# Performance work log

Hardware: AMD Instinct MI355X
Metric: run time of the kernel (lower is better)

## Reference

```python
import math
import jax, jax.numpy as jnp
import numpy as np

DIM = 1024
N_HEADS = 16
N_KV_HEADS = 4
HEAD_DIM = 64
WINDOW = 512
EPS = 1e-6
B, S = 2, 2048

def _alibi_slopes(n_heads):
    def pow2(n):
        r = 2.0 ** (-8.0 / n)
        return np.array([r ** (i + 1) for i in range(n)], dtype=np.float32)
    if math.log2(n_heads).is_integer():
        return pow2(n_heads)
    m = 2 ** math.floor(math.log2(n_heads))
    return np.concatenate([pow2(m), pow2(2 * m)[::2][: n_heads - m]])

def _rmsnorm(x, w, eps=EPS):
    var = jnp.mean(x * x, axis=-1, keepdims=True)
    return x * jax.lax.rsqrt(var + eps) * w

def setup_inputs() -> dict:
    key = jax.random.key(0)
    ks = jax.random.split(key, 8)
    x = jax.random.normal(ks[0], (B, S, DIM), dtype=jnp.float32)
    wq = 0.02 * jax.random.normal(ks[1], (N_HEADS * HEAD_DIM, DIM), dtype=jnp.float32)
    wk = 0.02 * jax.random.normal(ks[2], (N_KV_HEADS * HEAD_DIM, DIM), dtype=jnp.float32)
    wv = 0.02 * jax.random.normal(ks[3], (N_KV_HEADS * HEAD_DIM, DIM), dtype=jnp.float32)
    wo = 0.02 * jax.random.normal(ks[4], (DIM, N_HEADS * HEAD_DIM), dtype=jnp.float32)
    q_norm_w = jnp.ones((N_HEADS * HEAD_DIM,), dtype=jnp.float32)
    k_norm_w = jnp.ones((N_KV_HEADS * HEAD_DIM,), dtype=jnp.float32)
    return {"x": x, "wq": wq, "wk": wk, "wv": wv, "wo": wo,
            "q_norm_w": q_norm_w, "k_norm_w": k_norm_w}

def reference(x, wq, wk, wv, wo, q_norm_w, k_norm_w):
    bsz, seqlen, _ = x.shape
    repeats = N_HEADS // N_KV_HEADS
    xq = _rmsnorm(x @ wq.T, q_norm_w)
    xk = _rmsnorm(x @ wk.T, k_norm_w)
    xv = x @ wv.T
    # [b, h, s, d]
    q = xq.reshape(bsz, seqlen, N_HEADS, HEAD_DIM).transpose(0, 2, 1, 3)
    k = xk.reshape(bsz, seqlen, N_KV_HEADS, HEAD_DIM).transpose(0, 2, 1, 3)
    v = xv.reshape(bsz, seqlen, N_KV_HEADS, HEAD_DIM).transpose(0, 2, 1, 3)
    k = jnp.repeat(k, repeats, axis=1)
    v = jnp.repeat(v, repeats, axis=1)
    pos = jnp.arange(seqlen)
    rel = pos[None, :] - pos[:, None]  # [s_q, s_k], key - query
    slopes = jnp.asarray(_alibi_slopes(N_HEADS))
    bias = slopes[:, None, None] * rel[None].astype(x.dtype)  # [h, s, s]
    masked = (rel > 0) | (rel < -WINDOW)  # causal + sliding window
    bias = jnp.where(masked[None], -jnp.inf, bias)
    scale = 1.0 / math.sqrt(HEAD_DIM)
    scores = jnp.einsum('bhqd,bhkd->bhqk', q, k) * scale + bias[None]
    probs = jax.nn.softmax(scores, axis=-1)
    y = jnp.einsum('bhqk,bhkd->bhqd', probs, v)
    y = y.transpose(0, 2, 1, 3).reshape(bsz, seqlen, N_HEADS * HEAD_DIM)
    return y @ wo.T
```

## Files before the change

### kernel.cpp

```cpp
#include <hip/hip_runtime.h>

typedef unsigned short u16;
typedef unsigned int u32;

typedef __bf16 bf16x8 __attribute__((ext_vector_type(8)));
typedef float f32x4 __attribute__((ext_vector_type(4)));

__device__ __forceinline__ u16 f2bf(float f) {
  u32 u = __builtin_bit_cast(u32, f);
  u32 r = (u + 0x7fffu + ((u >> 16) & 1u)) >> 16;
  return (u16)r;
}
__device__ __forceinline__ float bf2f(u16 v) {
  u32 u = (u32)v << 16;
  return __builtin_bit_cast(float, u);
}

__global__ __launch_bounds__(256)
void cvt_all_kernel(const float* __restrict__ x, const float* __restrict__ wq,
                    const float* __restrict__ wk, const float* __restrict__ wv,
                    const float* __restrict__ wo, u16* __restrict__ x_bf,
                    u16* __restrict__ wcat_bf, u16* __restrict__ wo_bf) {
  int t = blockIdx.x * 256 + threadIdx.x;
  const float* src;
  u16* dst;
  if (t < 1048576) {
    src = x; dst = x_bf;
  } else if (t < 1310720) {
    src = wq; dst = wcat_bf; t -= 1048576;
  } else if (t < 1376256) {
    src = wk; dst = wcat_bf + 1048576; t -= 1310720;
  } else if (t < 1441792) {
    src = wv; dst = wcat_bf + 1310720; t -= 1376256;
  } else {
    src = wo; dst = wo_bf; t -= 1441792;
  }
  const int i = t * 4;
  float4 v = *(const float4*)(src + i);
  uint2 p;
  p.x = (u32)f2bf(v.x) | ((u32)f2bf(v.y) << 16);
  p.y = (u32)f2bf(v.z) | ((u32)f2bf(v.w) << 16);
  *(uint2*)(dst + i) = p;
}

template <typename OutT>
__global__ __launch_bounds__(256)
void gemm_bt_kernel(const u16* __restrict__ A, const u16* __restrict__ B,
                    OutT* __restrict__ C, int M, int N, int K) {
  __shared__ u16 As[64 * 64];
  __shared__ u16 Bs[128 * 64];
  const int tid = threadIdx.x;
  const int lane = tid & 63;
  const int wave = tid >> 6;
  const int wm = (wave >> 1) * 32;
  const int wn = (wave & 1) * 64;
  const int l15 = lane & 15;
  const int quad = lane >> 4;
  const int sw = l15 & 7;
  const size_t bm = (size_t)blockIdx.y * 64;
  const size_t bn = (size_t)blockIdx.x * 128;

  f32x4 acc[2][4];
#pragma unroll
  for (int i = 0; i < 2; ++i)
#pragma unroll
    for (int j = 0; j < 4; ++j) acc[i][j] = f32x4{0.f, 0.f, 0.f, 0.f};

  const int ra0 = tid >> 3, ba0 = tid & 7;
  const int ra1 = (tid + 256) >> 3, ba1 = tid & 7;
  const u16* Ap0 = A + (bm + ra0) * (size_t)K + ba0 * 8;
  const u16* Ap1 = A + (bm + ra1) * (size_t)K + ba1 * 8;
  const u16* Bp0 = B + (bn + ra0) * (size_t)K + ba0 * 8;
  const u16* Bp1 = B + (bn + ra1) * (size_t)K + ba1 * 8;
  const u16* Bp2 = B + (bn + ra0 + 64) * (size_t)K + ba0 * 8;
  const u16* Bp3 = B + (bn + ra1 + 64) * (size_t)K + ba1 * 8;
  const int wa0 = ra0 * 64 + ((ba0 ^ (ra0 & 7)) * 8);
  const int wa1 = ra1 * 64 + ((ba1 ^ (ra1 & 7)) * 8);
  const int wb2 = (ra0 + 64) * 64 + ((ba0 ^ (ra0 & 7)) * 8);
  const int wb3 = (ra1 + 64) * 64 + ((ba1 ^ (ra1 & 7)) * 8);

  uint4 a0 = *(const uint4*)Ap0, a1 = *(const uint4*)Ap1;
  uint4 b0 = *(const uint4*)Bp0, b1 = *(const uint4*)Bp1;
  uint4 b2 = *(const uint4*)Bp2, b3 = *(const uint4*)Bp3;

  for (int k0 = 0; k0 < K; k0 += 64) {
    __syncthreads();
    *(uint4*)(&As[wa0]) = a0;
    *(uint4*)(&As[wa1]) = a1;
    *(uint4*)(&Bs[wa0]) = b0;
    *(uint4*)(&Bs[wa1]) = b1;
    *(uint4*)(&Bs[wb2]) = b2;
    *(uint4*)(&Bs[wb3]) = b3;
    __syncthreads();
    const int kn = (k0 + 64 < K) ? k0 + 64 : 0;
    a0 = *(const uint4*)(Ap0 + kn);
    a1 = *(const uint4*)(Ap1 + kn);
    b0 = *(const uint4*)(Bp0 + kn);
    b1 = *(const uint4*)(Bp1 + kn);
    b2 = *(const uint4*)(Bp2 + kn);
    b3 = *(const uint4*)(Bp3 + kn);
#pragma unroll
    for (int h = 0; h < 2; ++h) {
      const int cb = (quad + 4 * h);
      bf16x8 af[2], bfr[4];
#pragma unroll
      for (int i = 0; i < 2; ++i)
        af[i] = *(const bf16x8*)(&As[(wm + i * 16 + l15) * 64 + ((cb ^ sw) * 8)]);
#pragma unroll
      for (int j = 0; j < 4; ++j)
        bfr[j] = *(const bf16x8*)(&Bs[(wn + j * 16 + l15) * 64 + ((cb ^ sw) * 8)]);
#pragma unroll
      for (int i = 0; i < 2; ++i)
#pragma unroll
        for (int j = 0; j < 4; ++j)
          acc[i][j] = __builtin_amdgcn_mfma_f32_16x16x32_bf16(af[i], bfr[j], acc[i][j], 0, 0, 0);
    }
  }

  const int rq = quad * 4;
#pragma unroll
  for (int i = 0; i < 2; ++i) {
#pragma unroll
    for (int r = 0; r < 4; ++r) {
      OutT* crow = C + (bm + wm + i * 16 + rq + r) * (size_t)N + bn + wn + l15;
#pragma unroll
      for (int j = 0; j < 4; ++j) {
        if constexpr (sizeof(OutT) == 2)
          crow[j * 16] = f2bf(acc[i][j][r]);
        else
          crow[j * 16] = acc[i][j][r];
      }
    }
  }
}

__global__ __launch_bounds__(256)
void norm_vtrans_kernel(u16* __restrict__ qkv, const float* __restrict__ qw,
                        const float* __restrict__ kw, u16* __restrict__ vt) {
  __shared__ u16 shmem[64 * 72];
  const int bid = blockIdx.x;
  const int tid = threadIdx.x;
  if (bid < 4096) {
    float* red = (float*)shmem;
    u16* row = qkv + (size_t)bid * 1536;
    uint2 pk = *(const uint2*)(row + tid * 4);
    float v0 = bf2f((u16)pk.x), v1 = bf2f((u16)(pk.x >> 16));
    float v2 = bf2f((u16)pk.y), v3 = bf2f((u16)(pk.y >> 16));
    float ss = v0 * v0 + v1 * v1 + v2 * v2 + v3 * v3;
#pragma unroll
    for (int off = 32; off > 0; off >>= 1) ss += __shfl_down(ss, off);
    if ((tid & 63) == 0) red[tid >> 6] = ss;
    __syncthreads();
    float tot = red[0] + red[1] + red[2] + red[3];
    float rn = rsqrtf(tot * (1.0f / 1024.0f) + 1e-6f);
    float4 w = *(const float4*)(qw + tid * 4);
    uint2 po;
    po.x = (u32)f2bf(v0 * rn * w.x) | ((u32)f2bf(v1 * rn * w.y) << 16);
    po.y = (u32)f2bf(v2 * rn * w.z) | ((u32)f2bf(v3 * rn * w.w) << 16);
    *(uint2*)(row + tid * 4) = po;
    if (tid < 64) {
      uint2 kp = *(const uint2*)(row + 1024 + tid * 4);
      float k0 = bf2f((u16)kp.x), k1 = bf2f((u16)(kp.x >> 16));
      float k2 = bf2f((u16)kp.y), k3 = bf2f((u16)(kp.y >> 16));
      float sk = k0 * k0 + k1 * k1 + k2 * k2 + k3 * k3;
#pragma unroll
      for (int off = 32; off > 0; off >>= 1) sk += __shfl_down(sk, off);
      float tk = __shfl(sk, 0);
      float rk = rsqrtf(tk * (1.0f / 256.0f) + 1e-6f);
      float4 w2 = *(const float4*)(kw + tid * 4);
      uint2 ko;
      ko.x = (u32)f2bf(k0 * rk * w2.x) | ((u32)f2bf(k1 * rk * w2.y) << 16);
      ko.y = (u32)f2bf(k2 * rk * w2.z) | ((u32)f2bf(k3 * rk * w2.w) << 16);
      *(uint2*)(row + 1024 + tid * 4) = ko;
    }
  } else {
    const int e = bid - 4096;
    const int t0 = (e & 31) * 64, kvh = (e >> 5) & 3, b = e >> 7;
    u16(*tile)[72] = (u16(*)[72])shmem;
    const int r = tid >> 2, c16 = (tid & 3) * 16;
    const u16* src = qkv + (size_t)(b * 2048 + t0 + r) * 1536 + 1280 + kvh * 64 + c16;
    *(uint4*)&tile[r][c16] = *(const uint4*)src;
    *(uint4*)&tile[r][c16 + 8] = *(const uint4*)(src + 8);
    __syncthreads();
    const int d = tid >> 2, t16 = (tid & 3) * 16;
    u16 o[16];
#pragma unroll
    for (int j = 0; j < 16; ++j) o[j] = tile[t16 + j][d];
    u16* dst = vt + (size_t)((b * 4 + kvh) * 64 + d) * 2048 + t0 + t16;
    *(uint4*)dst = *(uint4*)&o[0];
    *(uint4*)(dst + 8) = *(uint4*)&o[8];
  }
}

__global__ __launch_bounds__(512)
void attn_kernel(const u16* __restrict__ qkvbf, const u16* __restrict__ vt,
                 u16* __restrict__ ybf) {
  __shared__ u16 Ks[64 * 72];
  __shared__ u16 Vts[64 * 72];
  __shared__ u16 Ps[128 * 72];
  const int qt = blockIdx.x, h = blockIdx.y, b = blockIdx.z;
  const int kvh = h >> 2, q0 = qt * 128;
  const int tid = threadIdx.x, lane = tid & 63, w = tid >> 6;
  const int l15 = lane & 15, quad = lane >> 4;

  const u16* qrow = qkvbf + (size_t)(b * 2048 + q0 + w * 16 + l15) * 1536 + h * 64 + quad * 8;
  const bf16x8 qf0 = *(const bf16x8*)qrow;
  const bf16x8 qf1 = *(const bf16x8*)(qrow + 32);

  const int sr = tid >> 3, sc = (tid & 7) * 8;
  const u16* kbase = qkvbf + (size_t)(b * 2048 + sr) * 1536 + 1024 + kvh * 64 + sc;
  const u16* vbase = vt + (size_t)((b * 4 + kvh) * 64 + sr) * 2048 + sc;

  f32x4 O[4];
#pragma unroll
  for (int jd = 0; jd < 4; ++jd) O[jd] = f32x4{0.f, 0.f, 0.f, 0.f};
  float m_i = -1e30f, l_i = 0.f;
  const float LOG2E = 1.44269504f;
  const float sc2 = 0.125f * LOG2E;
  const float slope2 = exp2f(-0.5f * (float)(h + 1)) * LOG2E;
  const int c_lo = (q0 >= 512) ? (q0 - 512) : 0;
  const int c_hi = q0 + 64;
  const int myq_lo = q0 + w * 16;
  const int myq_hi = myq_lo + 15;
  const int myq = myq_lo + l15;

  uint4 kr = *(const uint4*)(kbase + (size_t)c_lo * 1536);
  uint4 vr = *(const uint4*)(vbase + c_lo);

  for (int c = c_lo; c <= c_hi; c += 64) {
    __syncthreads();
    *(uint4*)&Ks[sr * 72 + sc] = kr;
    *(uint4*)&Vts[sr * 72 + sc] = vr;
    __syncthreads();
    {
      const int cn = (c + 64 <= c_hi) ? c + 64 : c_lo;
      kr = *(const uint4*)(kbase + (size_t)cn * 1536);
      vr = *(const uint4*)(vbase + cn);
    }

    if (c > myq_hi || c + 63 < myq_lo - 512) continue;

    f32x4 st[4];
#pragma unroll
    for (int i = 0; i < 4; ++i) {
      bf16x8 a0 = *(const bf16x8*)&Ks[(i * 16 + l15) * 72 + quad * 8];
      bf16x8 a1 = *(const bf16x8*)&Ks[(i * 16 + l15) * 72 + 32 + quad * 8];
      f32x4 z = f32x4{0.f, 0.f, 0.f, 0.f};
      z = __builtin_amdgcn_mfma_f32_16x16x32_bf16(a0, qf0, z, 0, 0, 0);
      st[i] = __builtin_amdgcn_mfma_f32_16x16x32_bf16(a1, qf1, z, 0, 0, 0);
    }

    float sv[4][4];
    float rm = -1e30f;
    const bool interior = (c + 63 <= myq_lo) && (c + 512 >= myq_hi);
    if (interior) {
#pragma unroll
      for (int i = 0; i < 4; ++i)
#pragma unroll
        for (int r = 0; r < 4; ++r) {
          const int key = c + i * 16 + quad * 4 + r;
          float val = st[i][r] * sc2 + slope2 * (float)(key - myq);
          sv[i][r] = val;
          rm = fmaxf(rm, val);
        }
    } else {
#pragma unroll
      for (int i = 0; i < 4; ++i)
#pragma unroll
        for (int r = 0; r < 4; ++r) {
          const int key = c + i * 16 + quad * 4 + r;
          const int rel = key - myq;
          float val = (rel > 0 || rel < -512) ? -1e30f
                                              : st[i][r] * sc2 + slope2 * (float)rel;
          sv[i][r] = val;
          rm = fmaxf(rm, val);
        }
    }
    rm = fmaxf(rm, __shfl_xor(rm, 16));
    rm = fmaxf(rm, __shfl_xor(rm, 32));
    const float mn = fmaxf(m_i, rm);
    const float alpha = exp2f(m_i - mn);
    float ls = 0.f;
#pragma unroll
    for (int i = 0; i < 4; ++i) {
      float p0 = exp2f(sv[i][0] - mn);
      float p1 = exp2f(sv[i][1] - mn);
      float p2 = exp2f(sv[i][2] - mn);
      float p3 = exp2f(sv[i][3] - mn);
      ls += (p0 + p1) + (p2 + p3);
      uint2 pw;
      pw.x = (u32)f2bf(p0) | ((u32)f2bf(p1) << 16);
      pw.y = (u32)f2bf(p2) | ((u32)f2bf(p3) << 16);
      *(uint2*)&Ps[(w * 16 + l15) * 72 + i * 16 + quad * 4] = pw;
    }
    ls += __shfl_xor(ls, 16);
    ls += __shfl_xor(ls, 32);
    l_i = l_i * alpha + ls;
    m_i = mn;

    float ar[4];
#pragma unroll
    for (int r = 0; r < 4; ++r) ar[r] = __shfl(alpha, quad * 4 + r);
#pragma unroll
    for (int jd = 0; jd < 4; ++jd)
#pragma unroll
      for (int r = 0; r < 4; ++r) O[jd][r] *= ar[r];

    bf16x8 pf0 = *(const bf16x8*)&Ps[(w * 16 + l15) * 72 + quad * 8];
    bf16x8 pf1 = *(const bf16x8*)&Ps[(w * 16 + l15) * 72 + 32 + quad * 8];
#pragma unroll
    for (int jd = 0; jd < 4; ++jd) {
      bf16x8 v0 = *(const bf16x8*)&Vts[(jd * 16 + l15) * 72 + quad * 8];
      bf16x8 v1 = *(const bf16x8*)&Vts[(jd * 16 + l15) * 72 + 32 + quad * 8];
      O[jd] = __builtin_amdgcn_mfma_f32_16x16x32_bf16(pf0, v0, O[jd], 0, 0, 0);
      O[jd] = __builtin_amdgcn_mfma_f32_16x16x32_bf16(pf1, v1, O[jd], 0, 0, 0);
    }
  }

  float lr[4];
#pragma unroll
  for (int r = 0; r < 4; ++r) lr[r] = __shfl(l_i, quad * 4 + r);
#pragma unroll
  for (int r = 0; r < 4; ++r) {
    const float inv = 1.0f / lr[r];
    u16* orow = ybf + (size_t)(b * 2048 + q0 + w * 16 + quad * 4 + r) * 1024 + h * 64 + l15;
#pragma unroll
    for (int jd = 0; jd < 4; ++jd) orow[jd * 16] = f2bf(O[jd][r] * inv);
  }
}

extern "C" void kernel_launch(void* const* d_in, const int* in_sizes, int n_in,
                              void* d_out, int out_size, void* d_ws, size_t ws_size,
                              hipStream_t stream) {
  const float* x = (const float*)d_in[0];
  const float* wq = (const float*)d_in[1];
  const float* wk = (const float*)d_in[2];
  const float* wv = (const float*)d_in[3];
  const float* wo = (const float*)d_in[4];
  const float* qnw = (const float*)d_in[5];
  const float* knw = (const float*)d_in[6];
  float* out = (float*)d_out;
  char* ws = (char*)d_ws;

  u16* x_bf = (u16*)(ws);
  u16* wcat_bf = (u16*)(ws + 8388608);
  u16* wo_bf = (u16*)(ws + 11534336);
  u16* qkv_bf = (u16*)(ws + 13631488);
  u16* vt_bf = (u16*)(ws + 26214400);
  u16* y_bf = (u16*)(ws + 28311552);

  cvt_all_kernel<<<6656, 256, 0, stream>>>(x, wq, wk, wv, wo, x_bf, wcat_bf, wo_bf);

  gemm_bt_kernel<u16><<<dim3(12, 64), 256, 0, stream>>>(x_bf, wcat_bf, qkv_bf, 4096, 1536, 1024);
  norm_vtrans_kernel<<<4352, 256, 0, stream>>>(qkv_bf, qnw, knw, vt_bf);
  attn_kernel<<<dim3(16, 16, 2), 512, 0, stream>>>(qkv_bf, vt_bf, y_bf);
  gemm_bt_kernel<float><<<dim3(8, 64), 256, 0, stream>>>(y_bf, wo_bf, out, 4096, 1024, 1024);
}
```

Measured before the change: 160.3 us.

## Double-buffer shared memory tiles in GEMM and attention kernels

Both the GEMM and attention kernels now keep two LDS buffers for the operand tiles and use one barrier per iteration instead of two. The next tile is fetched from global memory, the current buffer is consumed by MFMA, and the fetched data is then written into the other buffer. The aim is to cut barrier overhead and overlap loads with compute. In exchange, LDS use doubles, which may lower occupancy, particularly for the attention kernel.

```diff
diff --git a/kernel.cpp b/kernel.cpp
--- a/kernel.cpp
+++ b/kernel.cpp
@@ -47,8 +47,8 @@
 __global__ __launch_bounds__(256)
 void gemm_bt_kernel(const u16* __restrict__ A, const u16* __restrict__ B,
                     OutT* __restrict__ C, int M, int N, int K) {
-  __shared__ u16 As[64 * 64];
-  __shared__ u16 Bs[128 * 64];
+  __shared__ u16 As[2][64 * 64];
+  __shared__ u16 Bs[2][128 * 64];
   const int tid = threadIdx.x;
   const int lane = tid & 63;
   const int wave = tid >> 6;
@@ -79,42 +79,58 @@
   const int wb2 = (ra0 + 64) * 64 + ((ba0 ^ (ra0 & 7)) * 8);
   const int wb3 = (ra1 + 64) * 64 + ((ba1 ^ (ra1 & 7)) * 8);
 
-  uint4 a0 = *(const uint4*)Ap0, a1 = *(const uint4*)Ap1;
-  uint4 b0 = *(const uint4*)Bp0, b1 = *(const uint4*)Bp1;
-  uint4 b2 = *(const uint4*)Bp2, b3 = *(const uint4*)Bp3;
-
+  {
+    uint4 a0 = *(const uint4*)Ap0, a1 = *(const uint4*)Ap1;
+    uint4 b0 = *(const uint4*)Bp0, b1 = *(const uint4*)Bp1;
+    uint4 b2 = *(const uint4*)Bp2, b3 = *(const uint4*)Bp3;
+    *(uint4*)(&As[0][wa0]) = a0;
+    *(uint4*)(&As[0][wa1]) = a1;
+    *(uint4*)(&Bs[0][wa0]) = b0;
+    *(uint4*)(&Bs[0][wa1]) = b1;
+    *(uint4*)(&Bs[0][wb2]) = b2;
+    *(uint4*)(&Bs[0][wb3]) = b3;
+  }
+  __syncthreads();
+
+  int cur = 0;
   for (int k0 = 0; k0 < K; k0 += 64) {
-    __syncthreads();
-    *(uint4*)(&As[wa0]) = a0;
-    *(uint4*)(&As[wa1]) = a1;
-    *(uint4*)(&Bs[wa0]) = b0;
-    *(uint4*)(&Bs[wa1]) = b1;
-    *(uint4*)(&Bs[wb2]) = b2;
-    *(uint4*)(&Bs[wb3]) = b3;
-    __syncthreads();
     const int kn = (k0 + 64 < K) ? k0 + 64 : 0;
-    a0 = *(const uint4*)(Ap0 + kn);
-    a1 = *(const uint4*)(Ap1 + kn);
-    b0 = *(const uint4*)(Bp0 + kn);
-    b1 = *(const uint4*)(Bp1 + kn);
-    b2 = *(const uint4*)(Bp2 + kn);
-    b3 = *(const uint4*)(Bp3 + kn);
+    uint4 a0 = *(const uint4*)(Ap0 + kn);
+    uint4 a1 = *(const uint4*)(Ap1 + kn);
+    uint4 b0 = *(const uint4*)(Bp0 + kn);
+    uint4 b1 = *(const uint4*)(Bp1 + kn);
+    uint4 b2 = *(const uint4*)(Bp2 + kn);
+    uint4 b3 = *(const uint4*)(Bp3 + kn);
+
+    const u16* Asc = As[cur];
+    const u16* Bsc = Bs[cur];
 #pragma unroll
     for (int h = 0; h < 2; ++h) {
-      const int cb = (quad + 4 * h);
+      const int cb = quad + 4 * h;
       bf16x8 af[2], bfr[4];
 #pragma unroll
       for (int i = 0; i < 2; ++i)
-        af[i] = *(const bf16x8*)(&As[(wm + i * 16 + l15) * 64 + ((cb ^ sw) * 8)]);
+        af[i] = *(const bf16x8*)(&Asc[(wm + i * 16 + l15) * 64 + ((cb ^ sw) * 8)]);
 #pragma unroll
       for (int j = 0; j < 4; ++j)
-        bfr[j] = *(const bf16x8*)(&Bs[(wn + j * 16 + l15) * 64 + ((cb ^ sw) * 8)]);
+        bfr[j] = *(const bf16x8*)(&Bsc[(wn + j * 16 + l15) * 64 + ((cb ^ sw) * 8)]);
 #pragma unroll
       for (int i = 0; i < 2; ++i)
 #pragma unroll
         for (int j = 0; j < 4; ++j)
           acc[i][j] = __builtin_amdgcn_mfma_f32_16x16x32_bf16(af[i], bfr[j], acc[i][j], 0, 0, 0);
     }
+
+    u16* Asn = As[cur ^ 1];
+    u16* Bsn = Bs[cur ^ 1];
+    *(uint4*)(&Asn[wa0]) = a0;
+    *(uint4*)(&Asn[wa1]) = a1;
+    *(uint4*)(&Bsn[wa0]) = b0;
+    *(uint4*)(&Bsn[wa1]) = b1;
+    *(uint4*)(&Bsn[wb2]) = b2;
+    *(uint4*)(&Bsn[wb3]) = b3;
+    __syncthreads();
+    cur ^= 1;
   }
 
   const int rq = quad * 4;
@@ -195,8 +211,8 @@
 __global__ __launch_bounds__(512)
 void attn_kernel(const u16* __restrict__ qkvbf, const u16* __restrict__ vt,
                  u16* __restrict__ ybf) {
-  __shared__ u16 Ks[64 * 72];
-  __shared__ u16 Vts[64 * 72];
+  __shared__ u16 Ks[2][64 * 72];
+  __shared__ u16 Vts[2][64 * 72];
   __shared__ u16 Ps[128 * 72];
   const int qt = blockIdx.x, h = blockIdx.y, b = blockIdx.z;
   const int kvh = h >> 2, q0 = qt * 128;
@@ -224,97 +240,104 @@
   const int myq_hi = myq_lo + 15;
   const int myq = myq_lo + l15;
 
-  uint4 kr = *(const uint4*)(kbase + (size_t)c_lo * 1536);
-  uint4 vr = *(const uint4*)(vbase + c_lo);
-
+  {
+    uint4 kr = *(const uint4*)(kbase + (size_t)c_lo * 1536);
+    uint4 vr = *(const uint4*)(vbase + c_lo);
+    *(uint4*)&Ks[0][sr * 72 + sc] = kr;
+    *(uint4*)&Vts[0][sr * 72 + sc] = vr;
+  }
+  __syncthreads();
+
+  int cur = 0;
   for (int c = c_lo; c <= c_hi; c += 64) {
+    const int cn = (c + 64 <= c_hi) ? c + 64 : c_lo;
+    uint4 kr = *(const uint4*)(kbase + (size_t)cn * 1536);
+    uint4 vr = *(const uint4*)(vbase + cn);
+
+    if (!(c > myq_hi || c + 63 < myq_lo - 512)) {
+      const u16* Kc = Ks[cur];
+      const u16* Vc = Vts[cur];
+      f32x4 st[4];
+#pragma unroll
+      for (int i = 0; i < 4; ++i) {
+        bf16x8 a0 = *(const bf16x8*)&Kc[(i * 16 + l15) * 72 + quad * 8];
+        bf16x8 a1 = *(const bf16x8*)&Kc[(i * 16 + l15) * 72 + 32 + quad * 8];
+        f32x4 z = f32x4{0.f, 0.f, 0.f, 0.f};
+        z = __builtin_amdgcn_mfma_f32_16x16x32_bf16(a0, qf0, z, 0, 0, 0);
+        st[i] = __builtin_amdgcn_mfma_f32_16x16x32_bf16(a1, qf1, z, 0, 0, 0);
+      }
+
+      float sv[4][4];
+      float rm = -1e30f;
+      const bool interior = (c + 63 <= myq_lo) && (c + 512 >= myq_hi);
+      if (interior) {
+#pragma unroll
+        for (int i = 0; i < 4; ++i)
+#pragma unroll
+          for (int r = 0; r < 4; ++r) {
+            const int key = c + i * 16 + quad * 4 + r;
+            float val = st[i][r] * sc2 + slope2 * (float)(key - myq);
+            sv[i][r] = val;
+            rm = fmaxf(rm, val);
+          }
+      } else {
+#pragma unroll
+        for (int i = 0; i < 4; ++i)
+#pragma unroll
+          for (int r = 0; r < 4; ++r) {
+            const int key = c + i * 16 + quad * 4 + r;
+            const int rel = key - myq;
+            float val = (rel > 0 || rel < -512) ? -1e30f
+                                                : st[i][r] * sc2 + slope2 * (float)rel;
+            sv[i][r] = val;
+            rm = fmaxf(rm, val);
+          }
+      }
+      rm = fmaxf(rm, __shfl_xor(rm, 16));
+      rm = fmaxf(rm, __shfl_xor(rm, 32));
+      const float mn = fmaxf(m_i, rm);
+      const float alpha = exp2f(m_i - mn);
+      float ls = 0.f;
+#pragma unroll
+      for (int i = 0; i < 4; ++i) {
+        float p0 = exp2f(sv[i][0] - mn);
+        float p1 = exp2f(sv[i][1] - mn);
+        float p2 = exp2f(sv[i][2] - mn);
+        float p3 = exp2f(sv[i][3] - mn);
+        ls += (p0 + p1) + (p2 + p3);
+        uint2 pw;
+        pw.x = (u32)f2bf(p0) | ((u32)f2bf(p1) << 16);
+        pw.y = (u32)f2bf(p2) | ((u32)f2bf(p3) << 16);
+        *(uint2*)&Ps[(w * 16 + l15) * 72 + i * 16 + quad * 4] = pw;
+      }
+      ls += __shfl_xor(ls, 16);
+      ls += __shfl_xor(ls, 32);
+      l_i = l_i * alpha + ls;
+      m_i = mn;
+
+      float ar[4];
+#pragma unroll
+      for (int r = 0; r < 4; ++r) ar[r] = __shfl(alpha, quad * 4 + r);
+#pragma unroll
+      for (int jd = 0; jd < 4; ++jd)
+#pragma unroll
+        for (int r = 0; r < 4; ++r) O[jd][r] *= ar[r];
+
+      bf16x8 pf0 = *(const bf16x8*)&Ps[(w * 16 + l15) * 72 + quad * 8];
+      bf16x8 pf1 = *(const bf16x8*)&Ps[(w * 16 + l15) * 72 + 32 + quad * 8];
+#pragma unroll
+      for (int jd = 0; jd < 4; ++jd) {
+        bf16x8 v0 = *(const bf16x8*)&Vc[(jd * 16 + l15) * 72 + quad * 8];
+        bf16x8 v1 = *(const bf16x8*)&Vc[(jd * 16 + l15) * 72 + 32 + quad * 8];
+        O[jd] = __builtin_amdgcn_mfma_f32_16x16x32_bf16(pf0, v0, O[jd], 0, 0, 0);
+        O[jd] = __builtin_amdgcn_mfma_f32_16x16x32_bf16(pf1, v1, O[jd], 0, 0, 0);
+      }
+    }
+
+    *(uint4*)&Ks[cur ^ 1][sr * 72 + sc] = kr;
+    *(uint4*)&Vts[cur ^ 1][sr * 72 + sc] = vr;
     __syncthreads();
-    *(uint4*)&Ks[sr * 72 + sc] = kr;
-    *(uint4*)&Vts[sr * 72 + sc] = vr;
-    __syncthreads();
-    {
-      const int cn = (c + 64 <= c_hi) ? c + 64 : c_lo;
-      kr = *(const uint4*)(kbase + (size_t)cn * 1536);
-      vr = *(const uint4*)(vbase + cn);
-    }
-
-    if (c > myq_hi || c + 63 < myq_lo - 512) continue;
-
-    f32x4 st[4];
-#pragma unroll
-    for (int i = 0; i < 4; ++i) {
-      bf16x8 a0 = *(const bf16x8*)&Ks[(i * 16 + l15) * 72 + quad * 8];
-      bf16x8 a1 = *(const bf16x8*)&Ks[(i * 16 + l15) * 72 + 32 + quad * 8];
-      f32x4 z = f32x4{0.f, 0.f, 0.f, 0.f};
-      z = __builtin_amdgcn_mfma_f32_16x16x32_bf16(a0, qf0, z, 0, 0, 0);
-      st[i] = __builtin_amdgcn_mfma_f32_16x16x32_bf16(a1, qf1, z, 0, 0, 0);
-    }
-
-    float sv[4][4];
-    float rm = -1e30f;
-    const bool interior = (c + 63 <= myq_lo) && (c + 512 >= myq_hi);
-    if (interior) {
-#pragma unroll
-      for (int i = 0; i < 4; ++i)
-#pragma unroll
-        for (int r = 0; r < 4; ++r) {
-          const int key = c + i * 16 + quad * 4 + r;
-          float val = st[i][r] * sc2 + slope2 * (float)(key - myq);
-          sv[i][r] = val;
-          rm = fmaxf(rm, val);
-        }
-    } else {
-#pragma unroll
-      for (int i = 0; i < 4; ++i)
-#pragma unroll
-        for (int r = 0; r < 4; ++r) {
-          const int key = c + i * 16 + quad * 4 + r;
-          const int rel = key - myq;
-          float val = (rel > 0 || rel < -512) ? -1e30f
-                                              : st[i][r] * sc2 + slope2 * (float)rel;
-          sv[i][r] = val;
-          rm = fmaxf(rm, val);
-        }
-    }
-    rm = fmaxf(rm, __shfl_xor(rm, 16));
-    rm = fmaxf(rm, __shfl_xor(rm, 32));
-    const float mn = fmaxf(m_i, rm);
-    const float alpha = exp2f(m_i - mn);
-    float ls = 0.f;
-#pragma unroll
-    for (int i = 0; i < 4; ++i) {
-      float p0 = exp2f(sv[i][0] - mn);
-      float p1 = exp2f(sv[i][1] - mn);
-      float p2 = exp2f(sv[i][2] - mn);
-      float p3 = exp2f(sv[i][3] - mn);
-      ls += (p0 + p1) + (p2 + p3);
-      uint2 pw;
-      pw.x = (u32)f2bf(p0) | ((u32)f2bf(p1) << 16);
-      pw.y = (u32)f2bf(p2) | ((u32)f2bf(p3) << 16);
-      *(uint2*)&Ps[(w * 16 + l15) * 72 + i * 16 + quad * 4] = pw;
-    }
-    ls += __shfl_xor(ls, 16);
-    ls += __shfl_xor(ls, 32);
-    l_i = l_i * alpha + ls;
-    m_i = mn;
-
-    float ar[4];
-#pragma unroll
-    for (int r = 0; r < 4; ++r) ar[r] = __shfl(alpha, quad * 4 + r);
-#pragma unroll
-    for (int jd = 0; jd < 4; ++jd)
-#pragma unroll
-      for (int r = 0; r < 4; ++r) O[jd][r] *= ar[r];
-
-    bf16x8 pf0 = *(const bf16x8*)&Ps[(w * 16 + l15) * 72 + quad * 8];
-    bf16x8 pf1 = *(const bf16x8*)&Ps[(w * 16 + l15) * 72 + 32 + quad * 8];
-#pragma unroll
-    for (int jd = 0; jd < 4; ++jd) {
-      bf16x8 v0 = *(const bf16x8*)&Vts[(jd * 16 + l15) * 72 + quad * 8];
-      bf16x8 v1 = *(const bf16x8*)&Vts[(jd * 16 + l15) * 72 + 32 + quad * 8];
-      O[jd] = __builtin_amdgcn_mfma_f32_16x16x32_bf16(pf0, v0, O[jd], 0, 0, 0);
-      O[jd] = __builtin_amdgcn_mfma_f32_16x16x32_bf16(pf1, v1, O[jd], 0, 0, 0);
-    }
+    cur ^= 1;
   }
 
   float lr[4];
```

Measured after the change: 160.3 us. No clear change (+0.0%).
